# Kernel tuning notes

Measured on AMD Instinct MI355X. Metric: run time of the kernel, lower is better.

The kernel has to match this reference:

```python
import jax, jax.numpy as jnp
import numpy as np
import math

MAPPING_LENGTH = 5
STRIDE = 2


def _up_last(x, L, s):
    """Zero-insert along last axis with stride s, sum L shifted copies,
    normalize by overlap count (0 -> 1), crop to length W*s."""
    W = x.shape[-1]
    # strided zero-insertion: values at positions 0, s, 2s, ...
    z = jnp.zeros(x.shape[:-1] + (W * s,), x.dtype).at[..., ::s].set(x)
    pad0 = [(0, 0)] * (x.ndim - 1)
    # sum of L shifted/padded copies (length W*s + L)
    acc = sum(jnp.pad(z, pad0 + [(k, L - k)]) for k in range(L))
    # normalization: how many source pixels land on each output position
    nz = jnp.zeros((W * s,), x.dtype).at[::s].set(jnp.ones((W,), x.dtype))
    nacc = sum(jnp.pad(nz, (k, L - k)) for k in range(L))
    norm = jnp.where(nacc == 0, jnp.ones_like(nacc), nacc)
    start = math.ceil(L / s) - 1
    return (acc / norm)[..., start:start + W * s]


def _up_w(x):
    return _up_last(x, MAPPING_LENGTH, STRIDE)


def _up_h(x):
    return jnp.swapaxes(_up_last(jnp.swapaxes(x, 2, 3), MAPPING_LENGTH, STRIDE), 2, 3)


def setup_inputs() -> dict:
    key = jax.random.key(0)
    k0, k1, k2 = jax.random.split(key, 3)
    return {
        "x0": jax.random.normal(k0, (8, 64, 64, 256), dtype=jnp.float32),
        "x1": jax.random.normal(k1, (8, 64, 128, 128), dtype=jnp.float32),
        "x2": jax.random.normal(k2, (8, 64, 256, 64), dtype=jnp.float32),
    }


def reference(x0, x1, x2):
    xs = [x0, x1, x2]
    out = []
    for x in xs:
        if len(out) > 0:
            out[-1] = (out[-1] + _up_w(x)) / 2
        if len(out) < len(xs) - 1:
            out.append(_up_h(x))
    return tuple(out)
```

## Files before the change

### kernel.cpp

```cpp
#include <hip/hip_runtime.h>


__device__ __forceinline__ float4 f4_add(float4 p, float4 q) {
    return make_float4(p.x + q.x, p.y + q.y, p.z + q.z, p.w + q.w);
}
__device__ __forceinline__ float4 f4_scale(float4 p, float s) {
    return make_float4(p.x * s, p.y * s, p.z * s, p.w * s);
}

__device__ __forceinline__ void upw8(float bm, float4 bq, float bp,
                                     bool first, bool last,
                                     float4& lo, float4& hi) {
    constexpr float THIRD = 1.0f / 3.0f;
    lo.x = first ? 0.5f * (bq.x + bq.y) : (bm + bq.x + bq.y) * THIRD;
    lo.y = 0.5f * (bq.x + bq.y);
    lo.z = (bq.x + bq.y + bq.z) * THIRD;
    lo.w = 0.5f * (bq.y + bq.z);
    hi.x = (bq.y + bq.z + bq.w) * THIRD;
    hi.y = 0.5f * (bq.z + bq.w);
    hi.z = last ? 0.5f * (bq.z + bq.w) : (bq.z + bq.w + bp) * THIRD;
    hi.w = last ? bq.w : 0.5f * (bq.w + bp);
}

template <int Ha, int Wo>
__device__ __forceinline__ void up_combine_body(
    const float* __restrict__ a,
    const float* __restrict__ b,
    float* __restrict__ out,
    int lin)
{
    constexpr int H2 = 2 * Ha;
    constexpr int Wb = Wo / 2;
    constexpr int T8 = Wo / 8;
    constexpr float THIRD = 1.0f / 3.0f;

    const int t = lin % T8;
    const int h = (lin / T8) % Ha;
    const int n = lin / (T8 * Ha);

    const float4* a4 = reinterpret_cast<const float4*>(a) + (size_t)n * Ha * (Wo / 4);
    const int c4 = 2 * t;
    float4 a0l = a4[(size_t)h * (Wo / 4) + c4];
    float4 a0h = a4[(size_t)h * (Wo / 4) + c4 + 1];
    float4 aml, amh, apl, aph;
    if (h > 0) {
        aml = a4[(size_t)(h - 1) * (Wo / 4) + c4];
        amh = a4[(size_t)(h - 1) * (Wo / 4) + c4 + 1];
    }
    if (h < Ha - 1) {
        apl = a4[(size_t)(h + 1) * (Wo / 4) + c4];
        aph = a4[(size_t)(h + 1) * (Wo / 4) + c4 + 1];
    }

    float4 evl, evh, odl, odh;
    if (h == 0) {
        evl = f4_scale(f4_add(a0l, apl), 0.5f);
        evh = f4_scale(f4_add(a0h, aph), 0.5f);
    } else if (h == Ha - 1) {
        evl = f4_scale(f4_add(aml, a0l), 0.5f);
        evh = f4_scale(f4_add(amh, a0h), 0.5f);
    } else {
        evl = f4_scale(f4_add(f4_add(aml, a0l), apl), THIRD);
        evh = f4_scale(f4_add(f4_add(amh, a0h), aph), THIRD);
    }
    if (h == Ha - 1) {
        odl = a0l; odh = a0h;
    } else {
        odl = f4_scale(f4_add(a0l, apl), 0.5f);
        odh = f4_scale(f4_add(a0h, aph), 0.5f);
    }

    const bool first = (t == 0), last = (t == T8 - 1);
    const float* brow0 = b + ((size_t)n * H2 + 2 * h) * Wb;
    const float* brow1 = brow0 + Wb;

    float4 bq0 = *reinterpret_cast<const float4*>(brow0 + 4 * t);
    float4 bq1 = *reinterpret_cast<const float4*>(brow1 + 4 * t);
    float bm0 = first ? 0.0f : brow0[4 * t - 1];
    float bm1 = first ? 0.0f : brow1[4 * t - 1];
    float bp0 = last ? 0.0f : brow0[4 * t + 4];
    float bp1 = last ? 0.0f : brow1[4 * t + 4];

    float4 w0l, w0h, w1l, w1h;
    upw8(bm0, bq0, bp0, first, last, w0l, w0h);
    upw8(bm1, bq1, bp1, first, last, w1l, w1h);

    float4* o4 = reinterpret_cast<float4*>(out) + ((size_t)n * H2 + 2 * h) * (Wo / 4) + c4;
    o4[0]          = f4_scale(f4_add(evl, w0l), 0.5f);
    o4[1]          = f4_scale(f4_add(evh, w0h), 0.5f);
    o4[Wo / 4]     = f4_scale(f4_add(odl, w1l), 0.5f);
    o4[Wo / 4 + 1] = f4_scale(f4_add(odh, w1h), 0.5f);
}

__global__ __launch_bounds__(256) void fused_up_kernel(
    const float* __restrict__ x0,
    const float* __restrict__ x1,
    const float* __restrict__ x2,
    float* __restrict__ out0,
    float* __restrict__ out1,
    int g0_blocks)
{
    if (blockIdx.x < (unsigned)g0_blocks) {
        const int lin = blockIdx.x * blockDim.x + threadIdx.x;
        up_combine_body<64, 256>(x0, x1, out0, lin);
    } else {
        const int lin = (blockIdx.x - g0_blocks) * blockDim.x + threadIdx.x;
        up_combine_body<128, 128>(x1, x2, out1, lin);
    }
}

extern "C" void kernel_launch(void* const* d_in, const int* in_sizes, int n_in,
                              void* d_out, int out_size, void* d_ws, size_t ws_size,
                              hipStream_t stream) {
    const float* x0 = (const float*)d_in[0];
    const float* x1 = (const float*)d_in[1];
    const float* x2 = (const float*)d_in[2];
    float* out = (float*)d_out;

    const int N = 8 * 64;
    float* out0 = out;
    float* out1 = out + (size_t)N * 128 * 256;

    const int g0 = (N * 64 * (256 / 8)) / 256;
    const int g1 = (N * 128 * (128 / 8)) / 256;
    dim3 grid(g0 + g1), block(256);
    hipLaunchKernelGGL(fused_up_kernel, grid, block, 0, stream,
                       x0, x1, x2, out0, out1, g0);
}
```

Baseline: 46.92 us.

## Process two source rows per thread, shuffle width halos, use nontemporal stores

Each thread now handles two rows of the coarser input and writes four output rows, so adjacent-row loads for the vertical upsample are shared between those rows. The thread count is halved to match. Neighbor values for the horizontal upsample now come from wavefront shuffles instead of extra scalar global loads. Output writes use nontemporal stores to avoid polluting the cache. The kernel is likely already near memory bandwidth, so the gain may be small, and the larger per-thread footprint raises register pressure.

```diff
diff --git a/kernel.cpp b/kernel.cpp
--- a/kernel.cpp
+++ b/kernel.cpp
@@ -1,5 +1,7 @@
 #include <hip/hip_runtime.h>
 
+
+typedef float vfloat4 __attribute__((ext_vector_type(4)));
 
 __device__ __forceinline__ float4 f4_add(float4 p, float4 q) {
     return make_float4(p.x + q.x, p.y + q.y, p.z + q.z, p.w + q.w);
@@ -22,6 +24,12 @@
     hi.w = last ? bq.w : 0.5f * (bq.w + bp);
 }
 
+__device__ __forceinline__ void store_nt(float4* p, float4 v) {
+    vfloat4 vv;
+    vv.x = v.x; vv.y = v.y; vv.z = v.z; vv.w = v.w;
+    __builtin_nontemporal_store(vv, reinterpret_cast<vfloat4*>(p));
+}
+
 template <int Ha, int Wo>
 __device__ __forceinline__ void up_combine_body(
     const float* __restrict__ a,
@@ -30,66 +38,64 @@
     int lin)
 {
     constexpr int H2 = 2 * Ha;
+    constexpr int HB = Ha / 2;
     constexpr int Wb = Wo / 2;
+    constexpr int W4 = Wo / 4;
     constexpr int T8 = Wo / 8;
     constexpr float THIRD = 1.0f / 3.0f;
 
-    const int t = lin % T8;
-    const int h = (lin / T8) % Ha;
-    const int n = lin / (T8 * Ha);
+    const int t  = lin % T8;
+    const int hb = (lin / T8) % HB;
+    const int n  = lin / (T8 * HB);
 
-    const float4* a4 = reinterpret_cast<const float4*>(a) + (size_t)n * Ha * (Wo / 4);
-    const int c4 = 2 * t;
-    float4 a0l = a4[(size_t)h * (Wo / 4) + c4];
-    float4 a0h = a4[(size_t)h * (Wo / 4) + c4 + 1];
+    const float4* a4 = reinterpret_cast<const float4*>(a)
+                     + (size_t)n * Ha * W4 + (size_t)(2 * hb) * W4 + 2 * t;
+    const bool htop = (hb == 0), hbot = (hb == HB - 1);
+    float4 a0l = a4[0],  a0h = a4[1];
+    float4 a1l = a4[W4], a1h = a4[W4 + 1];
     float4 aml, amh, apl, aph;
-    if (h > 0) {
-        aml = a4[(size_t)(h - 1) * (Wo / 4) + c4];
-        amh = a4[(size_t)(h - 1) * (Wo / 4) + c4 + 1];
-    }
-    if (h < Ha - 1) {
-        apl = a4[(size_t)(h + 1) * (Wo / 4) + c4];
-        aph = a4[(size_t)(h + 1) * (Wo / 4) + c4 + 1];
-    }
+    if (!htop) { aml = a4[-W4];     amh = a4[-W4 + 1]; }
+    if (!hbot) { apl = a4[2 * W4];  aph = a4[2 * W4 + 1]; }
 
-    float4 evl, evh, odl, odh;
-    if (h == 0) {
-        evl = f4_scale(f4_add(a0l, apl), 0.5f);
-        evh = f4_scale(f4_add(a0h, aph), 0.5f);
-    } else if (h == Ha - 1) {
-        evl = f4_scale(f4_add(aml, a0l), 0.5f);
-        evh = f4_scale(f4_add(amh, a0h), 0.5f);
-    } else {
-        evl = f4_scale(f4_add(f4_add(aml, a0l), apl), THIRD);
-        evh = f4_scale(f4_add(f4_add(amh, a0h), aph), THIRD);
-    }
-    if (h == Ha - 1) {
-        odl = a0l; odh = a0h;
-    } else {
-        odl = f4_scale(f4_add(a0l, apl), 0.5f);
-        odh = f4_scale(f4_add(a0h, aph), 0.5f);
-    }
+    float4 h0l, h0h, h1l, h1h, h2l, h2h, h3l, h3h;
+    float4 s01l = f4_add(a0l, a1l), s01h = f4_add(a0h, a1h);
+    h0l = htop ? f4_scale(s01l, 0.5f) : f4_scale(f4_add(aml, s01l), THIRD);
+    h0h = htop ? f4_scale(s01h, 0.5f) : f4_scale(f4_add(amh, s01h), THIRD);
+    h1l = f4_scale(s01l, 0.5f);
+    h1h = f4_scale(s01h, 0.5f);
+    h2l = hbot ? f4_scale(s01l, 0.5f) : f4_scale(f4_add(s01l, apl), THIRD);
+    h2h = hbot ? f4_scale(s01h, 0.5f) : f4_scale(f4_add(s01h, aph), THIRD);
+    h3l = hbot ? a1l : f4_scale(f4_add(a1l, apl), 0.5f);
+    h3h = hbot ? a1h : f4_scale(f4_add(a1h, aph), 0.5f);
 
     const bool first = (t == 0), last = (t == T8 - 1);
-    const float* brow0 = b + ((size_t)n * H2 + 2 * h) * Wb;
-    const float* brow1 = brow0 + Wb;
+    const float* brow = b + ((size_t)n * H2 + (size_t)(4 * hb)) * Wb + 4 * t;
+    float4 bq0 = *reinterpret_cast<const float4*>(brow);
+    float4 bq1 = *reinterpret_cast<const float4*>(brow + Wb);
+    float4 bq2 = *reinterpret_cast<const float4*>(brow + 2 * Wb);
+    float4 bq3 = *reinterpret_cast<const float4*>(brow + 3 * Wb);
 
-    float4 bq0 = *reinterpret_cast<const float4*>(brow0 + 4 * t);
-    float4 bq1 = *reinterpret_cast<const float4*>(brow1 + 4 * t);
-    float bm0 = first ? 0.0f : brow0[4 * t - 1];
-    float bm1 = first ? 0.0f : brow1[4 * t - 1];
-    float bp0 = last ? 0.0f : brow0[4 * t + 4];
-    float bp1 = last ? 0.0f : brow1[4 * t + 4];
+    float bm0 = __shfl_up(bq0.w, 1), bp0 = __shfl_down(bq0.x, 1);
+    float bm1 = __shfl_up(bq1.w, 1), bp1 = __shfl_down(bq1.x, 1);
+    float bm2 = __shfl_up(bq2.w, 1), bp2 = __shfl_down(bq2.x, 1);
+    float bm3 = __shfl_up(bq3.w, 1), bp3 = __shfl_down(bq3.x, 1);
 
-    float4 w0l, w0h, w1l, w1h;
+    float4 w0l, w0h, w1l, w1h, w2l, w2h, w3l, w3h;
     upw8(bm0, bq0, bp0, first, last, w0l, w0h);
     upw8(bm1, bq1, bp1, first, last, w1l, w1h);
+    upw8(bm2, bq2, bp2, first, last, w2l, w2h);
+    upw8(bm3, bq3, bp3, first, last, w3l, w3h);
 
-    float4* o4 = reinterpret_cast<float4*>(out) + ((size_t)n * H2 + 2 * h) * (Wo / 4) + c4;
-    o4[0]          = f4_scale(f4_add(evl, w0l), 0.5f);
-    o4[1]          = f4_scale(f4_add(evh, w0h), 0.5f);
-    o4[Wo / 4]     = f4_scale(f4_add(odl, w1l), 0.5f);
-    o4[Wo / 4 + 1] = f4_scale(f4_add(odh, w1h), 0.5f);
+    float4* o4 = reinterpret_cast<float4*>(out)
+               + ((size_t)n * H2 + (size_t)(4 * hb)) * W4 + 2 * t;
+    store_nt(o4 + 0,          f4_scale(f4_add(h0l, w0l), 0.5f));
+    store_nt(o4 + 1,          f4_scale(f4_add(h0h, w0h), 0.5f));
+    store_nt(o4 + W4,         f4_scale(f4_add(h1l, w1l), 0.5f));
+    store_nt(o4 + W4 + 1,     f4_scale(f4_add(h1h, w1h), 0.5f));
+    store_nt(o4 + 2 * W4,     f4_scale(f4_add(h2l, w2l), 0.5f));
+    store_nt(o4 + 2 * W4 + 1, f4_scale(f4_add(h2h, w2h), 0.5f));
+    store_nt(o4 + 3 * W4,     f4_scale(f4_add(h3l, w3l), 0.5f));
+    store_nt(o4 + 3 * W4 + 1, f4_scale(f4_add(h3h, w3h), 0.5f));
 }
 
 __global__ __launch_bounds__(256) void fused_up_kernel(
@@ -121,8 +127,8 @@
     float* out0 = out;
     float* out1 = out + (size_t)N * 128 * 256;
 
-    const int g0 = (N * 64 * (256 / 8)) / 256;
-    const int g1 = (N * 128 * (128 / 8)) / 256;
+    const int g0 = (N * (64 / 2) * (256 / 8)) / 256;
+    const int g1 = (N * (128 / 2) * (128 / 8)) / 256;
     dim3 grid(g0 + g1), block(256);
     hipLaunchKernelGGL(fused_up_kernel, grid, block, 0, stream,
                        x0, x1, x2, out0, out1, g0);
```

Result: slower. 68.76 us (+46.6%).
